# Performance work log

Hardware: AMD Instinct MI355X
Metric: run time of the kernel (lower is better)

Reference implementation:

```python
import jax, jax.numpy as jnp
import numpy as np

# Static config matching init_kwargs
H = 12            # num_heads
ALPHA = (1, 2, 3)
DEPTH = 5
BLOCK_DEPTH = 3
TOTAL_DEPTH_M1 = 14 - 1   # total_depth - 1
SMALL_ACTIVE = (BLOCK_DEPTH <= DEPTH <= TOTAL_DEPTH_M1 - BLOCK_DEPTH)  # True here


def _ln(x, g, b, eps=1e-5):
    m = jnp.mean(x, axis=-1, keepdims=True)
    v = jnp.mean((x - m) ** 2, axis=-1, keepdims=True)
    return (x - m) * jax.lax.rsqrt(v + eps) * g + b


def _attn_branch(xp, w_qkv, w_proj, b_proj, keep_heads, keep_ch):
    # xp: (B2, N, C). Heads >= keep_heads are zeroed in q,k,v (as in the torch
    # clone+zero), output channels >= keep_ch zeroed after proj.
    B2, N, C = xp.shape
    hd = C // H
    scale = hd ** -0.5
    qkv = (xp @ w_qkv).reshape(B2, N, 3, H, hd).transpose(2, 0, 3, 1, 4)  # (3,B2,H,N,hd)
    hmask = (jnp.arange(H) < keep_heads).astype(xp.dtype)[None, :, None, None]
    q, k, v = qkv[0] * hmask, qkv[1] * hmask, qkv[2] * hmask
    a = jax.nn.softmax(jnp.einsum('bhnd,bhmd->bhnm', q, k) * scale, axis=-1)
    o = jnp.einsum('bhnm,bhmd->bhnd', a, v).transpose(0, 2, 1, 3).reshape(B2, N, C)
    o = o @ w_proj + b_proj
    cmask = (jnp.arange(C) < keep_ch).astype(xp.dtype)
    return o * cmask


def _mlp_branch(xp, w1, b1, w2, b2, keep_ch):
    # Input channels >= keep_ch zeroed before fc1, output channels zeroed after fc2.
    C = xp.shape[-1]
    cmask = (jnp.arange(C) < keep_ch).astype(xp.dtype)
    h = jax.nn.gelu((xp * cmask) @ w1 + b1, approximate=False)  # torch nn.GELU exact
    return ((h @ w2) + b2) * cmask


def setup_inputs() -> dict:
    key = jax.random.key(0)
    ks = jax.random.split(key, 8)
    B, N, C = 64, 257, 768
    HID = 4 * C

    def w(k, shape):
        return jax.random.normal(k, shape, jnp.float32) * 0.02

    return {
        'x': jax.random.normal(ks[0], (B, N, C), jnp.float32),
        'gumbel_weights': jax.random.uniform(ks[1], (3,), jnp.float32),
        'n1l_g': jnp.ones((C,), jnp.float32), 'n1l_b': jnp.zeros((C,), jnp.float32),
        'n1s_g': jnp.ones((C,), jnp.float32), 'n1s_b': jnp.zeros((C,), jnp.float32),
        'w_qkv': w(ks[2], (C, 3 * C)),  # qkv_bias=False
        'w_proj': w(ks[3], (C, C)), 'b_proj': jnp.zeros((C,), jnp.float32),
        'n2l_g': jnp.ones((C,), jnp.float32), 'n2l_b': jnp.zeros((C,), jnp.float32),
        'n2s_g': jnp.ones((C,), jnp.float32), 'n2s_b': jnp.zeros((C,), jnp.float32),
        'w_fc1': w(ks[4], (C, HID)), 'b_fc1': jnp.zeros((HID,), jnp.float32),
        'w_fc2': w(ks[5], (HID, C)), 'b_fc2': jnp.zeros((C,), jnp.float32),
    }


def reference(x, gumbel_weights, n1l_g, n1l_b, n1s_g, n1s_b, w_qkv, w_proj, b_proj,
              n2l_g, n2l_b, n2s_g, n2s_b, w_fc1, b_fc1, w_fc2, b_fc2):
    B, N, C = x.shape
    B2 = B // 2

    # --- attention sub-block (pre-norm, residual) ---
    nl = _ln(x[:B2], n1l_g, n1l_b)
    ns = _ln(x[B2:], n1s_g, n1s_b)
    a_large = _attn_branch(nl, w_qkv, w_proj, b_proj, H, C)
    if SMALL_ACTIVE:
        a_small = sum(
            gumbel_weights[i] * _attn_branch(ns, w_qkv, w_proj, b_proj,
                                             H // ALPHA[i], C // ALPHA[i])
            for i in range(3))
        attn_out = jnp.concatenate([a_large, a_small], axis=0)
    else:
        attn_out = jnp.concatenate([a_large, a_large], axis=0)
    x = x + attn_out  # drop_path = Identity

    # --- mlp sub-block (pre-norm, residual) ---
    nl2 = _ln(x[:B2], n2l_g, n2l_b)
    ns2 = _ln(x[B2:], n2s_g, n2s_b)
    m_large = _mlp_branch(nl2, w_fc1, b_fc1, w_fc2, b_fc2, C)
    if SMALL_ACTIVE:
        m_small = sum(
            gumbel_weights[i] * _mlp_branch(ns2, w_fc1, b_fc1, w_fc2, b_fc2,
                                            C // ALPHA[i])
            for i in range(3))
        mlp_out = jnp.concatenate([m_large, m_small], axis=0)
    else:
        mlp_out = jnp.concatenate([m_large, m_large], axis=0)
    return x + mlp_out
```

## Files before the change

kernel.cpp:

```cpp
#include <hip/hip_runtime.h>
#include <hip/hip_bf16.h>

typedef short v8s __attribute__((ext_vector_type(8)));
typedef float v4f __attribute__((ext_vector_type(4)));

#define B2ROWS 8224
#define ROWS   16448

__device__ __forceinline__ float fast_gelu(float z) {
  float u = z * 0.70710678118654752f;
  float a = fabsf(u);
  float t = __builtin_amdgcn_rcpf(1.0f + 0.3275911f * a);
  float p = t * (0.254829592f + t * (-0.284496736f + t * (1.421413741f +
            t * (-1.453152027f + t * 1.061405429f))));
  float e = __expf(-a * a);
  float erfa = 1.0f - p * e;
  float erfu = copysignf(erfa, u);
  return 0.5f * z * (1.0f + erfu);
}

__global__ __launch_bounds__(256) void wprep(const float* __restrict__ W,
                                             __hip_bfloat16* __restrict__ Wt,
                                             int K, int N, int variant,
                                             const float* __restrict__ gw) {
  int k = blockIdx.x * 256 + threadIdx.x;
  int n = blockIdx.y;
  if (k >= K) return;
  float v = W[(size_t)k * N + n];
  if (variant == 1) {
    int h = k >> 6;
    float s = gw[0];
    if (h < 6 && n < 384) s += gw[1];
    if (h < 4 && n < 256) s += gw[2];
    v *= s;
  }
  Wt[(size_t)n * K + k] = __float2bfloat16(v);
}

__global__ void bias_prep(const float* __restrict__ bp, const float* __restrict__ b2,
                          const float* __restrict__ gw,
                          float* __restrict__ b_small, float* __restrict__ b2_small) {
  int c = blockIdx.x * 256 + threadIdx.x;
  if (c >= 768) return;
  float s = gw[0] + (c < 384 ? gw[1] : 0.f) + (c < 256 ? gw[2] : 0.f);
  b_small[c] = bp[c] * s;
  b2_small[c] = b2[c] * s;
}

__global__ __launch_bounds__(256) void ln_k(const float* __restrict__ X,
                                            __hip_bfloat16* __restrict__ out,
                                            const float* __restrict__ gl, const float* __restrict__ bl,
                                            const float* __restrict__ gs, const float* __restrict__ bs) {
  int wave = threadIdx.x >> 6, lane = threadIdx.x & 63;
  int row = blockIdx.x * 4 + wave;
  const float* g = (row < B2ROWS) ? gl : gs;
  const float* b = (row < B2ROWS) ? bl : bs;
  const float* xr = X + (size_t)row * 768;
  float v[12]; float s = 0.f, ss = 0.f;
#pragma unroll
  for (int i = 0; i < 12; i++) { v[i] = xr[lane + i * 64]; s += v[i]; ss += v[i] * v[i]; }
#pragma unroll
  for (int o = 32; o > 0; o >>= 1) { s += __shfl_xor(s, o, 64); ss += __shfl_xor(ss, o, 64); }
  float mean = s * (1.0f / 768.0f);
  float var = ss * (1.0f / 768.0f) - mean * mean;
  float rstd = rsqrtf(var + 1e-5f);
  __hip_bfloat16* orow = out + (size_t)row * 768;
#pragma unroll
  for (int i = 0; i < 12; i++) {
    int c = lane + i * 64;
    orow[c] = __float2bfloat16((v[i] - mean) * rstd * g[c] + b[c]);
  }
}

template<int FUSED>
__device__ __forceinline__ void gemm_body(
    const __hip_bfloat16* __restrict__ A, int lda,
    const __hip_bfloat16* __restrict__ Bt, int ldb,
    int M, int K,
    const float* __restrict__ bias,
    const float* __restrict__ resid, int ldr,
    const float* __restrict__ gw, int gidx,
    const __hip_bfloat16* __restrict__ addin,
    void* __restrict__ out, int ldo,
    int mode,
    __hip_bfloat16* __restrict__ aux1,
    __hip_bfloat16* __restrict__ aux2) {
  __shared__ __attribute__((aligned(16))) short Asm[3][128 * 32];
  __shared__ __attribute__((aligned(16))) short Bsm[3][128 * 32];
  int tid = threadIdx.x;
  int lane = tid & 63;
  int wave = tid >> 6;
  int wm = wave >> 1, wn = wave & 1;
  int l16 = lane & 15, quad = lane >> 4;

  int gx = gridDim.x;
  int nwg = gx * gridDim.y;
  int bid = blockIdx.y * gx + blockIdx.x;
  int q8 = nwg >> 3, r8 = nwg & 7;
  int xcd = bid & 7, lid = bid >> 3;
  int nb = (xcd < r8 ? xcd * (q8 + 1) : r8 * (q8 + 1) + (xcd - r8) * q8) + lid;
  int m0 = (nb / gx) * 128, n0 = (nb % gx) * 128;

  int sw = (quad ^ ((l16 >> 1) & 3)) * 8;

  const __hip_bfloat16* Ause = A;
  if (!FUSED && mode == 4) {
    if (n0 < 256) Ause = aux2;
    else if (n0 < 384) Ause = aux1;
    mode = 2;
  }

  int r4 = lane >> 2;
  int qs = (lane & 3) ^ ((r4 >> 1) & 3);

  const ushort* Au = (const ushort*)Ause;
  const ushort* Bu = (const ushort*)Bt;

  const ushort* agp[2];
  const ushort* bgp[2];
  int lof[2];
#pragma unroll
  for (int it = 0; it < 2; it++) {
    int rbase = wave * 16 + it * 64;
    int gr = m0 + rbase + r4; if (gr > M - 1) gr = M - 1;
    agp[it] = Au + (size_t)gr * lda + qs * 8;
    int gn = n0 + rbase + r4;
    bgp[it] = Bu + (size_t)gn * ldb + qs * 8;
    lof[it] = rbase * 32;
  }

  v4f acc[4][4];
#pragma unroll
  for (int i = 0; i < 4; i++)
#pragma unroll
    for (int j = 0; j < 4; j++) acc[i][j] = (v4f){0.f, 0.f, 0.f, 0.f};

  float bias4[4];
  float gw0 = 0.f, gw1 = 0.f, gw2 = 0.f;
  uint g1p[4][4][2], g2p[4][4][2];
  if constexpr (FUSED) {
    gw0 = gw[0]; gw1 = gw[1]; gw2 = gw[2];
#pragma unroll
    for (int j = 0; j < 4; j++) bias4[j] = bias[n0 + wn * 64 + j * 16 + l16];
  }

  auto snap = [&](uint (&gp)[4][4][2], float gwX) {
#pragma unroll
    for (int i = 0; i < 4; i++)
#pragma unroll
      for (int j = 0; j < 4; j++)
#pragma unroll
        for (int p = 0; p < 2; p++) {
          float v0 = gwX * fast_gelu(acc[i][j][2 * p] + bias4[j]);
          float v1 = gwX * fast_gelu(acc[i][j][2 * p + 1] + bias4[j]);
          __hip_bfloat16 h0 = __float2bfloat16(v0);
          __hip_bfloat16 h1 = __float2bfloat16(v1);
          gp[i][j][p] = ((uint)*(const ushort*)&h1 << 16) | (uint)*(const ushort*)&h0;
        }
  };

  auto stage = [&](int buf, int ko) {
#pragma unroll
    for (int it = 0; it < 2; it++) {
      __builtin_amdgcn_global_load_lds(
          (const __attribute__((address_space(1))) uint32_t*)(uintptr_t)(const void*)(agp[it] + ko),
          (__attribute__((address_space(3))) uint32_t*)(uint32_t)(uintptr_t)(const void*)&Asm[buf][lof[it]],
          16, 0, 0);
      __builtin_amdgcn_global_load_lds(
          (const __attribute__((address_space(1))) uint32_t*)(uintptr_t)(const void*)(bgp[it] + ko),
          (__attribute__((address_space(3))) uint32_t*)(uint32_t)(uintptr_t)(const void*)&Bsm[buf][lof[it]],
          16, 0, 0);
    }
  };

  int nk = K >> 5;
  stage(0, 0);
  stage(1, 32);

  int bc = 0;
  for (int t = 0; t < nk; ++t) {
    if constexpr (FUSED) {
      if (t == 8)  snap(g2p, gw2);
      if (t == 12) snap(g1p, gw1);
    }
    __builtin_amdgcn_sched_barrier(0);
    if (t + 1 < nk) {
      asm volatile("s_waitcnt vmcnt(4)" ::: "memory");
    } else {
      asm volatile("s_waitcnt vmcnt(0)" ::: "memory");
    }
    __builtin_amdgcn_s_barrier();
    __builtin_amdgcn_sched_barrier(0);
    if (t + 2 < nk) {
      int bsg = bc - 1; if (bsg < 0) bsg += 3;
      stage(bsg, (t + 2) * 32);
    }
    v8s af[4], bfr[4];
#pragma unroll
    for (int i = 0; i < 4; i++) af[i] = *(const v8s*)&Asm[bc][(wm * 64 + i * 16 + l16) * 32 + sw];
#pragma unroll
    for (int j = 0; j < 4; j++) bfr[j] = *(const v8s*)&Bsm[bc][(wn * 64 + j * 16 + l16) * 32 + sw];
#pragma unroll
    for (int i = 0; i < 4; i++)
#pragma unroll
      for (int j = 0; j < 4; j++)
        acc[i][j] = __builtin_amdgcn_mfma_f32_16x16x32_bf16(af[i], bfr[j], acc[i][j], 0, 0, 0);
    bc++; if (bc == 3) bc = 0;
  }

  if constexpr (FUSED) {
#pragma unroll
    for (int i = 0; i < 4; i++)
#pragma unroll
      for (int j = 0; j < 4; j++)
#pragma unroll
        for (int r = 0; r < 4; r++)
          acc[i][j][r] = gw0 * fast_gelu(acc[i][j][r] + bias4[j]);

    __syncthreads();
    ushort* S16 = (ushort*)(((wave < 2) ? (char*)Asm : (char*)Bsm) + (wave & 1) * 12288);

    auto flush = [&](void* dst) {
      asm volatile("s_waitcnt lgkmcnt(0)" ::: "memory");
#pragma unroll
      for (int i = 0; i < 4; i++)
#pragma unroll
        for (int j = 0; j < 4; j++)
#pragma unroll
          for (int r = 0; r < 4; r++) {
            __hip_bfloat16 hb = __float2bfloat16(acc[i][j][r]);
            S16[(i * 16 + quad * 4 + r) * 72 + j * 16 + l16] = *(const ushort*)&hb;
          }
      asm volatile("s_waitcnt lgkmcnt(0)" ::: "memory");
#pragma unroll
      for (int rr = 0; rr < 8; rr++) {
        int row = rr * 8 + (lane >> 3);
        int col0 = (lane & 7) * 8;
        int gr = m0 + wm * 64 + row;
        v8s val = *(const v8s*)&S16[row * 72 + col0];
        if (gr < M)
          *(v8s*)&((ushort*)dst)[(size_t)gr * ldo + (n0 + wn * 64 + col0)] = val;
      }
    };

    flush(out);
#pragma unroll
    for (int i = 0; i < 4; i++)
#pragma unroll
      for (int j = 0; j < 4; j++)
#pragma unroll
        for (int p = 0; p < 2; p++) {
          uint u = g1p[i][j][p];
          acc[i][j][2 * p]     += __uint_as_float(u << 16);
          acc[i][j][2 * p + 1] += __uint_as_float(u & 0xffff0000u);
        }
    flush(aux1);
#pragma unroll
    for (int i = 0; i < 4; i++)
#pragma unroll
      for (int j = 0; j < 4; j++)
#pragma unroll
        for (int p = 0; p < 2; p++) {
          uint u = g2p[i][j][p];
          acc[i][j][2 * p]     += __uint_as_float(u << 16);
          acc[i][j][2 * p + 1] += __uint_as_float(u & 0xffff0000u);
        }
    flush(aux2);
    return;
  } else {

  float scale = (gidx >= 0) ? gw[gidx] : 1.0f;

  __syncthreads();
  char* sbase = ((wave < 2) ? (char*)Asm : (char*)Bsm) + (wave & 1) * 12288;

  if (mode != 2) {
    ushort* S16 = (ushort*)sbase;
#pragma unroll
    for (int i = 0; i < 4; i++) {
#pragma unroll
      for (int j = 0; j < 4; j++) {
        int gc = n0 + wn * 64 + j * 16 + l16;
#pragma unroll
        for (int r = 0; r < 4; r++) {
          float v = acc[i][j][r];
          if (mode == 1) {
            float z = v + bias[gc];
            v = scale * fast_gelu(z);
          }
          __hip_bfloat16 hb = __float2bfloat16(v);
          S16[(i * 16 + quad * 4 + r) * 72 + j * 16 + l16] = *(const ushort*)&hb;
        }
      }
    }
    asm volatile("s_waitcnt lgkmcnt(0)" ::: "memory");
#pragma unroll
    for (int rr = 0; rr < 8; rr++) {
      int row = rr * 8 + (lane >> 3);
      int col0 = (lane & 7) * 8;
      int gr = m0 + wm * 64 + row;
      v8s val = *(const v8s*)&S16[row * 72 + col0];
      if (gr < M) {
        size_t go = (size_t)gr * ldo + (n0 + wn * 64 + col0);
        if (mode == 1 && addin) {
          v8s av = *(const v8s*)&((const ushort*)addin)[go];
#pragma unroll
          for (int e = 0; e < 8; e++) {
            float fv = __uint_as_float(((uint)(ushort)val[e]) << 16);
            float fa = __uint_as_float(((uint)(ushort)av[e]) << 16);
            __hip_bfloat16 hr = __float2bfloat16(fv + fa);
            val[e] = *(const short*)&hr;
          }
        }
        *(v8s*)&((ushort*)out)[go] = val;
      }
    }
  } else {
    float* S32 = (float*)sbase;
#pragma unroll
    for (int h = 0; h < 2; h++) {
      if (h) asm volatile("s_waitcnt lgkmcnt(0)" ::: "memory");
#pragma unroll
      for (int i = 0; i < 4; i++) {
#pragma unroll
        for (int jj = 0; jj < 2; jj++) {
          int j = h * 2 + jj;
          int gc = n0 + wn * 64 + j * 16 + l16;
#pragma unroll
          for (int r = 0; r < 4; r++)
            S32[(i * 16 + quad * 4 + r) * 36 + jj * 16 + l16] = acc[i][j][r] + bias[gc];
        }
      }
      asm volatile("s_waitcnt lgkmcnt(0)" ::: "memory");
#pragma unroll
      for (int rr = 0; rr < 8; rr++) {
        int row = rr * 8 + (lane >> 3);
        int c0 = (lane & 7) * 4;
        int gr = m0 + wm * 64 + row;
        v4f v = *(const v4f*)&S32[row * 36 + c0];
        if (gr < M) {
          int gc0 = n0 + wn * 64 + h * 32 + c0;
          v4f rv = *(const v4f*)&resid[(size_t)gr * ldr + gc0];
          v4f sres = v + rv;
          *(v4f*)&((float*)out)[(size_t)gr * ldo + gc0] = sres;
        }
      }
    }
  }
  }
}

__global__ __launch_bounds__(256) void gemm_k(
    const __hip_bfloat16* __restrict__ A, int lda,
    const __hip_bfloat16* __restrict__ Bt, int ldb,
    int M, int K,
    const float* __restrict__ bias,
    const float* __restrict__ resid, int ldr,
    const float* __restrict__ gw, int gidx,
    const __hip_bfloat16* __restrict__ addin,
    void* __restrict__ out, int ldo,
    int mode,
    __hip_bfloat16* __restrict__ aux1,
    __hip_bfloat16* __restrict__ aux2) {
  gemm_body<0>(A, lda, Bt, ldb, M, K, bias, resid, ldr, gw, gidx, addin,
               out, ldo, mode, aux1, aux2);
}

__global__ __launch_bounds__(256) void fc1f_k(
    const __hip_bfloat16* __restrict__ A, int lda,
    const __hip_bfloat16* __restrict__ Bt, int ldb,
    int M, int K,
    const float* __restrict__ bias,
    const float* __restrict__ gw,
    void* __restrict__ out, int ldo,
    __hip_bfloat16* __restrict__ outB,
    __hip_bfloat16* __restrict__ outC) {
  gemm_body<1>(A, lda, Bt, ldb, M, K, bias, nullptr, 0, gw, -1, nullptr,
               out, ldo, 3, outB, outC);
}

__global__ __launch_bounds__(256) void attn_k(const __hip_bfloat16* __restrict__ qkv,
                                              __hip_bfloat16* __restrict__ O) {
  __shared__ ushort Ks[64 * 72];
  __shared__ ushort Vs[64 * 64];
  __shared__ ushort Ps[4][16 * 72];
  int bh = blockIdx.x;
  int b = bh / 12, h = bh % 12;
  size_t base = (size_t)b * 257;
  const ushort* Qg = (const ushort*)qkv;
  int tid = threadIdx.x;
  int w = tid >> 6, lane = tid & 63;
  int l16 = lane & 15, quad = lane >> 4;
  int qrow0 = blockIdx.y * 64 + w * 16;

  v8s aq[2];
  {
    int gr = qrow0 + l16; if (gr > 256) gr = 256;
    const ushort* qp = Qg + (base + gr) * 2304 + h * 64;
    aq[0] = *(const v8s*)(qp + quad * 8);
    aq[1] = *(const v8s*)(qp + 32 + quad * 8);
  }

  float mrow[4], lrow[4];
  v4f o[4];
#pragma unroll
  for (int r = 0; r < 4; r++) { mrow[r] = -1e30f; lrow[r] = 0.f; }
#pragma unroll
  for (int dt = 0; dt < 4; dt++) o[dt] = (v4f){0.f, 0.f, 0.f, 0.f};

  for (int kt = 0; kt < 5; kt++) {
    __syncthreads();
#pragma unroll
    for (int it = 0; it < 2; it++) {
      int ch = tid + it * 256;
      int row = ch >> 3, oct = ch & 7;
      int gk = kt * 64 + row; if (gk > 256) gk = 256;
      *(uint4*)&Ks[row * 72 + oct * 8] =
        *(const uint4*)(Qg + (base + gk) * 2304 + 768 + h * 64 + oct * 8);
    }
#pragma unroll
    for (int it = 0; it < 2; it++) {
      int oct = w + it * 4;
      int gk = kt * 64 + lane; if (gk > 256) gk = 256;
      ushort tmp[8];
      *(uint4*)tmp = *(const uint4*)(Qg + (base + gk) * 2304 + 1536 + h * 64 + oct * 8);
#pragma unroll
      for (int j = 0; j < 8; j++) {
        int d = oct * 8 + j;
        Vs[d * 64 + (((lane >> 3) ^ j) * 8) + (lane & 7)] = tmp[j];
      }
    }
    __syncthreads();

    v4f s[4];
#pragma unroll
    for (int jt = 0; jt < 4; jt++) {
      v8s bk0 = *(const v8s*)&Ks[(jt * 16 + l16) * 72 + quad * 8];
      v8s bk1 = *(const v8s*)&Ks[(jt * 16 + l16) * 72 + 32 + quad * 8];
      v4f acc = (v4f){0.f, 0.f, 0.f, 0.f};
      acc = __builtin_amdgcn_mfma_f32_16x16x32_bf16(aq[0], bk0, acc, 0, 0, 0);
      acc = __builtin_amdgcn_mfma_f32_16x16x32_bf16(aq[1], bk1, acc, 0, 0, 0);
      s[jt] = acc;
    }
#pragma unroll
    for (int jt = 0; jt < 4; jt++) {
      int col = kt * 64 + jt * 16 + l16;
      bool valid = col < 257;
#pragma unroll
      for (int r = 0; r < 4; r++)
        s[jt][r] = valid ? s[jt][r] * 0.125f : -1e30f;
    }
    float mnew[4], alpha[4], psum[4];
#pragma unroll
    for (int r = 0; r < 4; r++) {
      float mx = fmaxf(fmaxf(s[0][r], s[1][r]), fmaxf(s[2][r], s[3][r]));
#pragma unroll
      for (int off = 1; off < 16; off <<= 1) mx = fmaxf(mx, __shfl_xor(mx, off, 64));
      mnew[r] = fmaxf(mrow[r], mx);
      alpha[r] = __expf(mrow[r] - mnew[r]);
      mrow[r] = mnew[r];
      psum[r] = 0.f;
    }
#pragma unroll
    for (int jt = 0; jt < 4; jt++) {
#pragma unroll
      for (int r = 0; r < 4; r++) {
        float p = __expf(s[jt][r] - mnew[r]);
        psum[r] += p;
        __hip_bfloat16 pb = __float2bfloat16(p);
        Ps[w][(quad * 4 + r) * 72 + jt * 16 + l16] = *(ushort*)&pb;
      }
    }
#pragma unroll
    for (int r = 0; r < 4; r++) {
#pragma unroll
      for (int off = 1; off < 16; off <<= 1) psum[r] += __shfl_xor(psum[r], off, 64);
      lrow[r] = lrow[r] * alpha[r] + psum[r];
    }
#pragma unroll
    for (int dt = 0; dt < 4; dt++)
#pragma unroll
      for (int r = 0; r < 4; r++) o[dt][r] *= alpha[r];
    v8s pa0 = *(const v8s*)&Ps[w][l16 * 72 + quad * 8];
    v8s pa1 = *(const v8s*)&Ps[w][l16 * 72 + 32 + quad * 8];
#pragma unroll
    for (int dt = 0; dt < 4; dt++) {
      int d = dt * 16 + l16;
      v8s bv0 = *(const v8s*)&Vs[d * 64 + ((quad ^ (d & 7)) * 8)];
      v8s bv1 = *(const v8s*)&Vs[d * 64 + (((4 + quad) ^ (d & 7)) * 8)];
      o[dt] = __builtin_amdgcn_mfma_f32_16x16x32_bf16(pa0, bv0, o[dt], 0, 0, 0);
      o[dt] = __builtin_amdgcn_mfma_f32_16x16x32_bf16(pa1, bv1, o[dt], 0, 0, 0);
    }
  }
#pragma unroll
  for (int r = 0; r < 4; r++) {
    int gr = qrow0 + quad * 4 + r;
    if (gr < 257) {
      float inv = 1.f / lrow[r];
      __hip_bfloat16* orow = O + (base + gr) * 768 + h * 64;
#pragma unroll
      for (int dt = 0; dt < 4; dt++)
        orow[dt * 16 + l16] = __float2bfloat16(o[dt][r] * inv);
    }
  }
}

extern "C" void kernel_launch(void* const* d_in, const int* in_sizes, int n_in,
                              void* d_out, int out_size, void* d_ws, size_t ws_size,
                              hipStream_t stream) {
  const float* x      = (const float*)d_in[0];
  const float* gw     = (const float*)d_in[1];
  const float* n1l_g  = (const float*)d_in[2];
  const float* n1l_b  = (const float*)d_in[3];
  const float* n1s_g  = (const float*)d_in[4];
  const float* n1s_b  = (const float*)d_in[5];
  const float* w_qkv  = (const float*)d_in[6];
  const float* w_proj = (const float*)d_in[7];
  const float* b_proj = (const float*)d_in[8];
  const float* n2l_g  = (const float*)d_in[9];
  const float* n2l_b  = (const float*)d_in[10];
  const float* n2s_g  = (const float*)d_in[11];
  const float* n2s_b  = (const float*)d_in[12];
  const float* w_fc1  = (const float*)d_in[13];
  const float* b_fc1  = (const float*)d_in[14];
  const float* w_fc2  = (const float*)d_in[15];
  const float* b_fc2  = (const float*)d_in[16];
  float* out = (float*)d_out;

  const size_t REQUIRED = (size_t)(2304*768 + 2*768*768 + 2*3072*768) * 2
                        + 2 * 768 * 4 + 512
                        + (size_t)ROWS * 768 * 2
                        + (size_t)ROWS * 2304 * 2;
  if (ws_size < REQUIRED) return;

  char* ws = (char*)d_ws;
  size_t off = 0;
  auto alloc = [&](size_t bytes) -> void* {
    void* p = ws + off;
    off = (off + bytes + 255) & ~(size_t)255;
    return p;
  };
  __hip_bfloat16* wqkv_t  = (__hip_bfloat16*)alloc((size_t)2304 * 768 * 2);
  __hip_bfloat16* wproj_l = (__hip_bfloat16*)alloc((size_t)768 * 768 * 2);
  __hip_bfloat16* wproj_s = (__hip_bfloat16*)alloc((size_t)768 * 768 * 2);
  __hip_bfloat16* wfc1_t  = (__hip_bfloat16*)alloc((size_t)3072 * 768 * 2);
  __hip_bfloat16* wfc2_t  = (__hip_bfloat16*)alloc((size_t)768 * 3072 * 2);
  float* b_small  = (float*)alloc(768 * 4);
  float* b2_small = (float*)alloc(768 * 4);
  __hip_bfloat16* xn   = (__hip_bfloat16*)alloc((size_t)ROWS * 768 * 2);
  __hip_bfloat16* qkv  = (__hip_bfloat16*)alloc((size_t)ROWS * 2304 * 2);
  __hip_bfloat16* Obuf = xn;
  __hip_bfloat16* xn2  = qkv;
  __hip_bfloat16* hbuf = qkv + (size_t)ROWS * 768;

  const size_t HB2 = (size_t)B2ROWS * 3072 * 2;
  bool roomy = ws_size >= REQUIRED + 2 * HB2 + 512;
  __hip_bfloat16 *outB = nullptr, *outC = nullptr;
  if (roomy) {
    outB = (__hip_bfloat16*)alloc(HB2);
    outC = (__hip_bfloat16*)alloc(HB2);
  }

  wprep<<<dim3(3, 2304), 256, 0, stream>>>(w_qkv, wqkv_t, 768, 2304, 0, gw);
  wprep<<<dim3(3, 768),  256, 0, stream>>>(w_proj, wproj_l, 768, 768, 0, gw);
  wprep<<<dim3(3, 768),  256, 0, stream>>>(w_proj, wproj_s, 768, 768, 1, gw);
  wprep<<<dim3(3, 3072), 256, 0, stream>>>(w_fc1, wfc1_t, 768, 3072, 0, gw);
  wprep<<<dim3(12, 768), 256, 0, stream>>>(w_fc2, wfc2_t, 3072, 768, 0, gw);
  bias_prep<<<3, 256, 0, stream>>>(b_proj, b_fc2, gw, b_small, b2_small);

  ln_k<<<ROWS / 4, 256, 0, stream>>>(x, xn, n1l_g, n1l_b, n1s_g, n1s_b);

  gemm_k<<<dim3(18, 129), 256, 0, stream>>>(xn, 768, wqkv_t, 768, ROWS, 768,
                                            nullptr, nullptr, 0, gw, -1, nullptr,
                                            qkv, 2304, 0, nullptr, nullptr);
  attn_k<<<dim3(768, 5), 256, 0, stream>>>(qkv, Obuf);

  gemm_k<<<dim3(6, 65), 256, 0, stream>>>(Obuf, 768, wproj_l, 768, B2ROWS, 768,
                                          b_proj, x, 768, gw, -1, nullptr, out, 768, 2,
                                          nullptr, nullptr);
  gemm_k<<<dim3(6, 65), 256, 0, stream>>>(Obuf + (size_t)B2ROWS * 768, 768, wproj_s, 768, B2ROWS, 768,
                                          b_small, x + (size_t)B2ROWS * 768, 768, gw, -1, nullptr,
                                          out + (size_t)B2ROWS * 768, 768, 2, nullptr, nullptr);

  ln_k<<<ROWS / 4, 256, 0, stream>>>(out, xn2, n2l_g, n2l_b, n2s_g, n2s_b);
  const __hip_bfloat16* xn2s = xn2 + (size_t)B2ROWS * 768;
  float* outs = out + (size_t)B2ROWS * 768;

  gemm_k<<<dim3(24, 65), 256, 0, stream>>>(xn2, 768, wfc1_t, 768, B2ROWS, 768,
                                           b_fc1, nullptr, 0, gw, -1, nullptr, hbuf, 3072, 1,
                                           nullptr, nullptr);
  gemm_k<<<dim3(6, 65), 256, 0, stream>>>(hbuf, 3072, wfc2_t, 3072, B2ROWS, 3072,
                                          b_fc2, out, 768, gw, -1, nullptr, out, 768, 2,
                                          nullptr, nullptr);

  if (roomy) {
    fc1f_k<<<dim3(24, 65), 256, 0, stream>>>(xn2s, 768, wfc1_t, 768, B2ROWS, 768,
                                             b_fc1, gw, hbuf, 3072, outB, outC);
    gemm_k<<<dim3(6, 65), 256, 0, stream>>>(hbuf, 3072, wfc2_t, 3072, B2ROWS, 3072,
                                            b2_small, outs, 768, gw, -1, nullptr, outs, 768, 4,
                                            outB, outC);
  } else {
    gemm_k<<<dim3(24, 65), 256, 0, stream>>>(xn2s, 768, wfc1_t, 768, B2ROWS, 768,
                                             b_fc1, nullptr, 0, gw, 0, nullptr, hbuf, 3072, 1,
                                             nullptr, nullptr);
    gemm_k<<<dim3(3, 65), 256, 0, stream>>>(hbuf, 3072, wfc2_t + (size_t)384 * 3072, 3072, B2ROWS, 3072,
                                            b2_small + 384, outs + 384, 768, gw, -1, nullptr, outs + 384, 768, 2,
                                            nullptr, nullptr);
    gemm_k<<<dim3(24, 65), 256, 0, stream>>>(xn2s, 768, wfc1_t, 768, B2ROWS, 384,
                                             b_fc1, nullptr, 0, gw, 1, hbuf, hbuf, 3072, 1,
                                             nullptr, nullptr);
    gemm_k<<<dim3(1, 65), 256, 0, stream>>>(hbuf, 3072, wfc2_t + (size_t)256 * 3072, 3072, B2ROWS, 3072,
                                            b2_small + 256, outs + 256, 768, gw, -1, nullptr, outs + 256, 768, 2,
                                            nullptr, nullptr);
    gemm_k<<<dim3(24, 65), 256, 0, stream>>>(xn2s, 768, wfc1_t, 768, B2ROWS, 256,
                                             b_fc1, nullptr, 0, gw, 2, hbuf, hbuf, 3072, 1,
                                             nullptr, nullptr);
    gemm_k<<<dim3(2, 65), 256, 0, stream>>>(hbuf, 3072, wfc2_t, 3072, B2ROWS, 3072,
                                            b2_small, outs, 768, gw, -1, nullptr, outs, 768, 2,
                                            nullptr, nullptr);
  }
}
```

Baseline: 745.2 us.

## Merge proj GEMMs into one launch and shrink fused fc1 tile width

The two attention output projection GEMMs (large and small branches) become a single launch with a new mode that picks the A, weight, bias, residual and output pointers from the row block index. This removes one launch and the tail effect between them. The fused fc1 kernel that keeps three GELU-scaled snapshots now uses 128x64 tiles instead of 128x128, which halves the accumulator and snapshot registers and doubles the grid. The aim is better occupancy and less register pressure, at the cost of lower reuse of each A tile.

Result: faster. 726.6 us (-2.5%).

```diff
diff --git a/kernel.cpp b/kernel.cpp
--- a/kernel.cpp
+++ b/kernel.cpp
@@ -2,6 +2,7 @@
 #include <hip/hip_bf16.h>
 
 typedef short v8s __attribute__((ext_vector_type(8)));
+typedef short v4s __attribute__((ext_vector_type(4)));
 typedef float v4f __attribute__((ext_vector_type(4)));
 
 #define B2ROWS 8224
@@ -72,284 +73,6 @@
   }
 }
 
-template<int FUSED>
-__device__ __forceinline__ void gemm_body(
-    const __hip_bfloat16* __restrict__ A, int lda,
-    const __hip_bfloat16* __restrict__ Bt, int ldb,
-    int M, int K,
-    const float* __restrict__ bias,
-    const float* __restrict__ resid, int ldr,
-    const float* __restrict__ gw, int gidx,
-    const __hip_bfloat16* __restrict__ addin,
-    void* __restrict__ out, int ldo,
-    int mode,
-    __hip_bfloat16* __restrict__ aux1,
-    __hip_bfloat16* __restrict__ aux2) {
-  __shared__ __attribute__((aligned(16))) short Asm[3][128 * 32];
-  __shared__ __attribute__((aligned(16))) short Bsm[3][128 * 32];
-  int tid = threadIdx.x;
-  int lane = tid & 63;
-  int wave = tid >> 6;
-  int wm = wave >> 1, wn = wave & 1;
-  int l16 = lane & 15, quad = lane >> 4;
-
-  int gx = gridDim.x;
-  int nwg = gx * gridDim.y;
-  int bid = blockIdx.y * gx + blockIdx.x;
-  int q8 = nwg >> 3, r8 = nwg & 7;
-  int xcd = bid & 7, lid = bid >> 3;
-  int nb = (xcd < r8 ? xcd * (q8 + 1) : r8 * (q8 + 1) + (xcd - r8) * q8) + lid;
-  int m0 = (nb / gx) * 128, n0 = (nb % gx) * 128;
-
-  int sw = (quad ^ ((l16 >> 1) & 3)) * 8;
-
-  const __hip_bfloat16* Ause = A;
-  if (!FUSED && mode == 4) {
-    if (n0 < 256) Ause = aux2;
-    else if (n0 < 384) Ause = aux1;
-    mode = 2;
-  }
-
-  int r4 = lane >> 2;
-  int qs = (lane & 3) ^ ((r4 >> 1) & 3);
-
-  const ushort* Au = (const ushort*)Ause;
-  const ushort* Bu = (const ushort*)Bt;
-
-  const ushort* agp[2];
-  const ushort* bgp[2];
-  int lof[2];
-#pragma unroll
-  for (int it = 0; it < 2; it++) {
-    int rbase = wave * 16 + it * 64;
-    int gr = m0 + rbase + r4; if (gr > M - 1) gr = M - 1;
-    agp[it] = Au + (size_t)gr * lda + qs * 8;
-    int gn = n0 + rbase + r4;
-    bgp[it] = Bu + (size_t)gn * ldb + qs * 8;
-    lof[it] = rbase * 32;
-  }
-
-  v4f acc[4][4];
-#pragma unroll
-  for (int i = 0; i < 4; i++)
-#pragma unroll
-    for (int j = 0; j < 4; j++) acc[i][j] = (v4f){0.f, 0.f, 0.f, 0.f};
-
-  float bias4[4];
-  float gw0 = 0.f, gw1 = 0.f, gw2 = 0.f;
-  uint g1p[4][4][2], g2p[4][4][2];
-  if constexpr (FUSED) {
-    gw0 = gw[0]; gw1 = gw[1]; gw2 = gw[2];
-#pragma unroll
-    for (int j = 0; j < 4; j++) bias4[j] = bias[n0 + wn * 64 + j * 16 + l16];
-  }
-
-  auto snap = [&](uint (&gp)[4][4][2], float gwX) {
-#pragma unroll
-    for (int i = 0; i < 4; i++)
-#pragma unroll
-      for (int j = 0; j < 4; j++)
-#pragma unroll
-        for (int p = 0; p < 2; p++) {
-          float v0 = gwX * fast_gelu(acc[i][j][2 * p] + bias4[j]);
-          float v1 = gwX * fast_gelu(acc[i][j][2 * p + 1] + bias4[j]);
-          __hip_bfloat16 h0 = __float2bfloat16(v0);
-          __hip_bfloat16 h1 = __float2bfloat16(v1);
-          gp[i][j][p] = ((uint)*(const ushort*)&h1 << 16) | (uint)*(const ushort*)&h0;
-        }
-  };
-
-  auto stage = [&](int buf, int ko) {
-#pragma unroll
-    for (int it = 0; it < 2; it++) {
-      __builtin_amdgcn_global_load_lds(
-          (const __attribute__((address_space(1))) uint32_t*)(uintptr_t)(const void*)(agp[it] + ko),
-          (__attribute__((address_space(3))) uint32_t*)(uint32_t)(uintptr_t)(const void*)&Asm[buf][lof[it]],
-          16, 0, 0);
-      __builtin_amdgcn_global_load_lds(
-          (const __attribute__((address_space(1))) uint32_t*)(uintptr_t)(const void*)(bgp[it] + ko),
-          (__attribute__((address_space(3))) uint32_t*)(uint32_t)(uintptr_t)(const void*)&Bsm[buf][lof[it]],
-          16, 0, 0);
-    }
-  };
-
-  int nk = K >> 5;
-  stage(0, 0);
-  stage(1, 32);
-
-  int bc = 0;
-  for (int t = 0; t < nk; ++t) {
-    if constexpr (FUSED) {
-      if (t == 8)  snap(g2p, gw2);
-      if (t == 12) snap(g1p, gw1);
-    }
-    __builtin_amdgcn_sched_barrier(0);
-    if (t + 1 < nk) {
-      asm volatile("s_waitcnt vmcnt(4)" ::: "memory");
-    } else {
-      asm volatile("s_waitcnt vmcnt(0)" ::: "memory");
-    }
-    __builtin_amdgcn_s_barrier();
-    __builtin_amdgcn_sched_barrier(0);
-    if (t + 2 < nk) {
-      int bsg = bc - 1; if (bsg < 0) bsg += 3;
-      stage(bsg, (t + 2) * 32);
-    }
-    v8s af[4], bfr[4];
-#pragma unroll
-    for (int i = 0; i < 4; i++) af[i] = *(const v8s*)&Asm[bc][(wm * 64 + i * 16 + l16) * 32 + sw];
-#pragma unroll
-    for (int j = 0; j < 4; j++) bfr[j] = *(const v8s*)&Bsm[bc][(wn * 64 + j * 16 + l16) * 32 + sw];
-#pragma unroll
-    for (int i = 0; i < 4; i++)
-#pragma unroll
-      for (int j = 0; j < 4; j++)
-        acc[i][j] = __builtin_amdgcn_mfma_f32_16x16x32_bf16(af[i], bfr[j], acc[i][j], 0, 0, 0);
-    bc++; if (bc == 3) bc = 0;
-  }
-
-  if constexpr (FUSED) {
-#pragma unroll
-    for (int i = 0; i < 4; i++)
-#pragma unroll
-      for (int j = 0; j < 4; j++)
-#pragma unroll
-        for (int r = 0; r < 4; r++)
-          acc[i][j][r] = gw0 * fast_gelu(acc[i][j][r] + bias4[j]);
-
-    __syncthreads();
-    ushort* S16 = (ushort*)(((wave < 2) ? (char*)Asm : (char*)Bsm) + (wave & 1) * 12288);
-
-    auto flush = [&](void* dst) {
-      asm volatile("s_waitcnt lgkmcnt(0)" ::: "memory");
-#pragma unroll
-      for (int i = 0; i < 4; i++)
-#pragma unroll
-        for (int j = 0; j < 4; j++)
-#pragma unroll
-          for (int r = 0; r < 4; r++) {
-            __hip_bfloat16 hb = __float2bfloat16(acc[i][j][r]);
-            S16[(i * 16 + quad * 4 + r) * 72 + j * 16 + l16] = *(const ushort*)&hb;
-          }
-      asm volatile("s_waitcnt lgkmcnt(0)" ::: "memory");
-#pragma unroll
-      for (int rr = 0; rr < 8; rr++) {
-        int row = rr * 8 + (lane >> 3);
-        int col0 = (lane & 7) * 8;
-        int gr = m0 + wm * 64 + row;
-        v8s val = *(const v8s*)&S16[row * 72 + col0];
-        if (gr < M)
-          *(v8s*)&((ushort*)dst)[(size_t)gr * ldo + (n0 + wn * 64 + col0)] = val;
-      }
-    };
-
-    flush(out);
-#pragma unroll
-    for (int i = 0; i < 4; i++)
-#pragma unroll
-      for (int j = 0; j < 4; j++)
-#pragma unroll
-        for (int p = 0; p < 2; p++) {
-          uint u = g1p[i][j][p];
-          acc[i][j][2 * p]     += __uint_as_float(u << 16);
-          acc[i][j][2 * p + 1] += __uint_as_float(u & 0xffff0000u);
-        }
-    flush(aux1);
-#pragma unroll
-    for (int i = 0; i < 4; i++)
-#pragma unroll
-      for (int j = 0; j < 4; j++)
-#pragma unroll
-        for (int p = 0; p < 2; p++) {
-          uint u = g2p[i][j][p];
-          acc[i][j][2 * p]     += __uint_as_float(u << 16);
-          acc[i][j][2 * p + 1] += __uint_as_float(u & 0xffff0000u);
-        }
-    flush(aux2);
-    return;
-  } else {
-
-  float scale = (gidx >= 0) ? gw[gidx] : 1.0f;
-
-  __syncthreads();
-  char* sbase = ((wave < 2) ? (char*)Asm : (char*)Bsm) + (wave & 1) * 12288;
-
-  if (mode != 2) {
-    ushort* S16 = (ushort*)sbase;
-#pragma unroll
-    for (int i = 0; i < 4; i++) {
-#pragma unroll
-      for (int j = 0; j < 4; j++) {
-        int gc = n0 + wn * 64 + j * 16 + l16;
-#pragma unroll
-        for (int r = 0; r < 4; r++) {
-          float v = acc[i][j][r];
-          if (mode == 1) {
-            float z = v + bias[gc];
-            v = scale * fast_gelu(z);
-          }
-          __hip_bfloat16 hb = __float2bfloat16(v);
-          S16[(i * 16 + quad * 4 + r) * 72 + j * 16 + l16] = *(const ushort*)&hb;
-        }
-      }
-    }
-    asm volatile("s_waitcnt lgkmcnt(0)" ::: "memory");
-#pragma unroll
-    for (int rr = 0; rr < 8; rr++) {
-      int row = rr * 8 + (lane >> 3);
-      int col0 = (lane & 7) * 8;
-      int gr = m0 + wm * 64 + row;
-      v8s val = *(const v8s*)&S16[row * 72 + col0];
-      if (gr < M) {
-        size_t go = (size_t)gr * ldo + (n0 + wn * 64 + col0);
-        if (mode == 1 && addin) {
-          v8s av = *(const v8s*)&((const ushort*)addin)[go];
-#pragma unroll
-          for (int e = 0; e < 8; e++) {
-            float fv = __uint_as_float(((uint)(ushort)val[e]) << 16);
-            float fa = __uint_as_float(((uint)(ushort)av[e]) << 16);
-            __hip_bfloat16 hr = __float2bfloat16(fv + fa);
-            val[e] = *(const short*)&hr;
-          }
-        }
-        *(v8s*)&((ushort*)out)[go] = val;
-      }
-    }
-  } else {
-    float* S32 = (float*)sbase;
-#pragma unroll
-    for (int h = 0; h < 2; h++) {
-      if (h) asm volatile("s_waitcnt lgkmcnt(0)" ::: "memory");
-#pragma unroll
-      for (int i = 0; i < 4; i++) {
-#pragma unroll
-        for (int jj = 0; jj < 2; jj++) {
-          int j = h * 2 + jj;
-          int gc = n0 + wn * 64 + j * 16 + l16;
-#pragma unroll
-          for (int r = 0; r < 4; r++)
-            S32[(i * 16 + quad * 4 + r) * 36 + jj * 16 + l16] = acc[i][j][r] + bias[gc];
-        }
-      }
-      asm volatile("s_waitcnt lgkmcnt(0)" ::: "memory");
-#pragma unroll
-      for (int rr = 0; rr < 8; rr++) {
-        int row = rr * 8 + (lane >> 3);
-        int c0 = (lane & 7) * 4;
-        int gr = m0 + wm * 64 + row;
-        v4f v = *(const v4f*)&S32[row * 36 + c0];
-        if (gr < M) {
-          int gc0 = n0 + wn * 64 + h * 32 + c0;
-          v4f rv = *(const v4f*)&resid[(size_t)gr * ldr + gc0];
-          v4f sres = v + rv;
-          *(v4f*)&((float*)out)[(size_t)gr * ldo + gc0] = sres;
-        }
-      }
-    }
-  }
-  }
-}
-
 __global__ __launch_bounds__(256) void gemm_k(
     const __hip_bfloat16* __restrict__ A, int lda,
     const __hip_bfloat16* __restrict__ Bt, int ldb,
@@ -360,10 +83,196 @@
     const __hip_bfloat16* __restrict__ addin,
     void* __restrict__ out, int ldo,
     int mode,
-    __hip_bfloat16* __restrict__ aux1,
-    __hip_bfloat16* __restrict__ aux2) {
-  gemm_body<0>(A, lda, Bt, ldb, M, K, bias, resid, ldr, gw, gidx, addin,
-               out, ldo, mode, aux1, aux2);
+    const __hip_bfloat16* __restrict__ aux1,
+    const __hip_bfloat16* __restrict__ aux2,
+    const float* __restrict__ bias2) {
+  __shared__ __attribute__((aligned(16))) short Asm[3][128 * 32];
+  __shared__ __attribute__((aligned(16))) short Bsm[3][128 * 32];
+  int tid = threadIdx.x;
+  int lane = tid & 63;
+  int wave = tid >> 6;
+  int wm = wave >> 1, wn = wave & 1;
+  int l16 = lane & 15, quad = lane >> 4;
+
+  int gx = gridDim.x;
+  int nwg = gx * gridDim.y;
+  int bid = blockIdx.y * gx + blockIdx.x;
+  int q8 = nwg >> 3, r8 = nwg & 7;
+  int xcd = bid & 7, lid = bid >> 3;
+  int nb = (xcd < r8 ? xcd * (q8 + 1) : r8 * (q8 + 1) + (xcd - r8) * q8) + lid;
+  int m0 = (nb / gx) * 128, n0 = (nb % gx) * 128;
+
+  int sw = (quad ^ ((l16 >> 1) & 3)) * 8;
+
+  const __hip_bfloat16* Ause = A;
+  const __hip_bfloat16* Btuse = Bt;
+  const float* bias_u = bias;
+  const float* resid_u = resid;
+  void* out_u = out;
+  if (mode == 4) {
+    if (n0 < 256) Ause = aux2;
+    else if (n0 < 384) Ause = aux1;
+    mode = 2;
+  } else if (mode == 5) {
+    if (m0 >= 8320) {
+      m0 -= 8320;
+      Ause = A + (size_t)B2ROWS * lda;
+      Btuse = aux1;
+      bias_u = bias2;
+      resid_u = resid + (size_t)B2ROWS * ldr;
+      out_u = (void*)((float*)out + (size_t)B2ROWS * ldo);
+    }
+    mode = 2;
+  }
+
+  int r4 = lane >> 2;
+  int qs = (lane & 3) ^ ((r4 >> 1) & 3);
+
+  const ushort* Au = (const ushort*)Ause;
+  const ushort* Bu = (const ushort*)Btuse;
+
+  const ushort* agp[2];
+  const ushort* bgp[2];
+  int lof[2];
+#pragma unroll
+  for (int it = 0; it < 2; it++) {
+    int rbase = wave * 16 + it * 64;
+    int gr = m0 + rbase + r4; if (gr > M - 1) gr = M - 1;
+    agp[it] = Au + (size_t)gr * lda + qs * 8;
+    int gn = n0 + rbase + r4;
+    bgp[it] = Bu + (size_t)gn * ldb + qs * 8;
+    lof[it] = rbase * 32;
+  }
+
+  v4f acc[4][4];
+#pragma unroll
+  for (int i = 0; i < 4; i++)
+#pragma unroll
+    for (int j = 0; j < 4; j++) acc[i][j] = (v4f){0.f, 0.f, 0.f, 0.f};
+
+  auto stage = [&](int buf, int ko) {
+#pragma unroll
+    for (int it = 0; it < 2; it++) {
+      __builtin_amdgcn_global_load_lds(
+          (const __attribute__((address_space(1))) uint32_t*)(uintptr_t)(const void*)(agp[it] + ko),
+          (__attribute__((address_space(3))) uint32_t*)(uint32_t)(uintptr_t)(const void*)&Asm[buf][lof[it]],
+          16, 0, 0);
+      __builtin_amdgcn_global_load_lds(
+          (const __attribute__((address_space(1))) uint32_t*)(uintptr_t)(const void*)(bgp[it] + ko),
+          (__attribute__((address_space(3))) uint32_t*)(uint32_t)(uintptr_t)(const void*)&Bsm[buf][lof[it]],
+          16, 0, 0);
+    }
+  };
+
+  int nk = K >> 5;
+  stage(0, 0);
+  stage(1, 32);
+
+  int bc = 0;
+  for (int t = 0; t < nk; ++t) {
+    __builtin_amdgcn_sched_barrier(0);
+    if (t + 1 < nk) {
+      asm volatile("s_waitcnt vmcnt(4)" ::: "memory");
+    } else {
+      asm volatile("s_waitcnt vmcnt(0)" ::: "memory");
+    }
+    __builtin_amdgcn_s_barrier();
+    __builtin_amdgcn_sched_barrier(0);
+    if (t + 2 < nk) {
+      int bsg = bc - 1; if (bsg < 0) bsg += 3;
+      stage(bsg, (t + 2) * 32);
+    }
+    v8s af[4], bfr[4];
+#pragma unroll
+    for (int i = 0; i < 4; i++) af[i] = *(const v8s*)&Asm[bc][(wm * 64 + i * 16 + l16) * 32 + sw];
+#pragma unroll
+    for (int j = 0; j < 4; j++) bfr[j] = *(const v8s*)&Bsm[bc][(wn * 64 + j * 16 + l16) * 32 + sw];
+#pragma unroll
+    for (int i = 0; i < 4; i++)
+#pragma unroll
+      for (int j = 0; j < 4; j++)
+        acc[i][j] = __builtin_amdgcn_mfma_f32_16x16x32_bf16(af[i], bfr[j], acc[i][j], 0, 0, 0);
+    bc++; if (bc == 3) bc = 0;
+  }
+
+  float scale = (gidx >= 0) ? gw[gidx] : 1.0f;
+
+  __syncthreads();
+  char* sbase = ((wave < 2) ? (char*)Asm : (char*)Bsm) + (wave & 1) * 12288;
+
+  if (mode != 2) {
+    ushort* S16 = (ushort*)sbase;
+#pragma unroll
+    for (int i = 0; i < 4; i++) {
+#pragma unroll
+      for (int j = 0; j < 4; j++) {
+        int gc = n0 + wn * 64 + j * 16 + l16;
+#pragma unroll
+        for (int r = 0; r < 4; r++) {
+          float v = acc[i][j][r];
+          if (mode == 1) {
+            float z = v + bias_u[gc];
+            v = scale * fast_gelu(z);
+          }
+          __hip_bfloat16 hb = __float2bfloat16(v);
+          S16[(i * 16 + quad * 4 + r) * 72 + j * 16 + l16] = *(const ushort*)&hb;
+        }
+      }
+    }
+    asm volatile("s_waitcnt lgkmcnt(0)" ::: "memory");
+#pragma unroll
+    for (int rr = 0; rr < 8; rr++) {
+      int row = rr * 8 + (lane >> 3);
+      int col0 = (lane & 7) * 8;
+      int gr = m0 + wm * 64 + row;
+      v8s val = *(const v8s*)&S16[row * 72 + col0];
+      if (gr < M) {
+        size_t go = (size_t)gr * ldo + (n0 + wn * 64 + col0);
+        if (mode == 1 && addin) {
+          v8s av = *(const v8s*)&((const ushort*)addin)[go];
+#pragma unroll
+          for (int e = 0; e < 8; e++) {
+            float fv = __uint_as_float(((uint)(ushort)val[e]) << 16);
+            float fa = __uint_as_float(((uint)(ushort)av[e]) << 16);
+            __hip_bfloat16 hr = __float2bfloat16(fv + fa);
+            val[e] = *(const short*)&hr;
+          }
+        }
+        *(v8s*)&((ushort*)out_u)[go] = val;
+      }
+    }
+  } else {
+    float* S32 = (float*)sbase;
+#pragma unroll
+    for (int h = 0; h < 2; h++) {
+      if (h) asm volatile("s_waitcnt lgkmcnt(0)" ::: "memory");
+#pragma unroll
+      for (int i = 0; i < 4; i++) {
+#pragma unroll
+        for (int jj = 0; jj < 2; jj++) {
+          int j = h * 2 + jj;
+          int gc = n0 + wn * 64 + j * 16 + l16;
+#pragma unroll
+          for (int r = 0; r < 4; r++)
+            S32[(i * 16 + quad * 4 + r) * 36 + jj * 16 + l16] = acc[i][j][r] + bias_u[gc];
+        }
+      }
+      asm volatile("s_waitcnt lgkmcnt(0)" ::: "memory");
+#pragma unroll
+      for (int rr = 0; rr < 8; rr++) {
+        int row = rr * 8 + (lane >> 3);
+        int c0 = (lane & 7) * 4;
+        int gr = m0 + wm * 64 + row;
+        v4f v = *(const v4f*)&S32[row * 36 + c0];
+        if (gr < M) {
+          int gc0 = n0 + wn * 64 + h * 32 + c0;
+          v4f rv = *(const v4f*)&resid_u[(size_t)gr * ldr + gc0];
+          v4f sres = v + rv;
+          *(v4f*)&((float*)out_u)[(size_t)gr * ldo + gc0] = sres;
+        }
+      }
+    }
+  }
 }
 
 __global__ __launch_bounds__(256) void fc1f_k(
@@ -375,8 +284,166 @@
     void* __restrict__ out, int ldo,
     __hip_bfloat16* __restrict__ outB,
     __hip_bfloat16* __restrict__ outC) {
-  gemm_body<1>(A, lda, Bt, ldb, M, K, bias, nullptr, 0, gw, -1, nullptr,
-               out, ldo, 3, outB, outC);
+  __shared__ __attribute__((aligned(16))) short As2[3][128 * 32];
+  __shared__ __attribute__((aligned(16))) short Bs2[3][64 * 32];
+  int tid = threadIdx.x, lane = tid & 63, wave = tid >> 6;
+  int wm = wave >> 1, wn = wave & 1;
+  int l16 = lane & 15, quad = lane >> 4;
+
+  int gx = gridDim.x;
+  int nwg = gx * gridDim.y;
+  int bid = blockIdx.y * gx + blockIdx.x;
+  int q8 = nwg >> 3, r8 = nwg & 7;
+  int xcd = bid & 7, lid = bid >> 3;
+  int nb = (xcd < r8 ? xcd * (q8 + 1) : r8 * (q8 + 1) + (xcd - r8) * q8) + lid;
+  int m0 = (nb / gx) * 128, n0 = (nb % gx) * 64;
+
+  int sw = (quad ^ ((l16 >> 1) & 3)) * 8;
+  int r4 = lane >> 2;
+  int qs = (lane & 3) ^ ((r4 >> 1) & 3);
+
+  const ushort* Au = (const ushort*)A;
+  const ushort* Bu = (const ushort*)Bt;
+  const ushort* agp[2];
+#pragma unroll
+  for (int it = 0; it < 2; it++) {
+    int gr = m0 + wave * 16 + it * 64 + r4; if (gr > M - 1) gr = M - 1;
+    agp[it] = Au + (size_t)gr * lda + qs * 8;
+  }
+  const ushort* bgp = Bu + (size_t)(n0 + wave * 16 + r4) * ldb + qs * 8;
+
+  v4f acc[4][2];
+#pragma unroll
+  for (int i = 0; i < 4; i++)
+#pragma unroll
+    for (int j = 0; j < 2; j++) acc[i][j] = (v4f){0.f, 0.f, 0.f, 0.f};
+
+  float gw0 = gw[0], gw1 = gw[1], gw2 = gw[2];
+  float bias2r[2];
+#pragma unroll
+  for (int j = 0; j < 2; j++) bias2r[j] = bias[n0 + wn * 32 + j * 16 + l16];
+
+  uint g1p[4][2][2], g2p[4][2][2];
+
+  auto snap = [&](uint (&gp)[4][2][2], float gwX) {
+#pragma unroll
+    for (int i = 0; i < 4; i++)
+#pragma unroll
+      for (int j = 0; j < 2; j++)
+#pragma unroll
+        for (int p = 0; p < 2; p++) {
+          float v0 = gwX * fast_gelu(acc[i][j][2 * p] + bias2r[j]);
+          float v1 = gwX * fast_gelu(acc[i][j][2 * p + 1] + bias2r[j]);
+          __hip_bfloat16 h0 = __float2bfloat16(v0);
+          __hip_bfloat16 h1 = __float2bfloat16(v1);
+          gp[i][j][p] = ((uint)*(const ushort*)&h1 << 16) | (uint)*(const ushort*)&h0;
+        }
+  };
+
+  auto stage = [&](int buf, int ko) {
+#pragma unroll
+    for (int it = 0; it < 2; it++) {
+      __builtin_amdgcn_global_load_lds(
+          (const __attribute__((address_space(1))) uint32_t*)(uintptr_t)(const void*)(agp[it] + ko),
+          (__attribute__((address_space(3))) uint32_t*)(uint32_t)(uintptr_t)(const void*)&As2[buf][(wave * 16 + it * 64) * 32],
+          16, 0, 0);
+    }
+    __builtin_amdgcn_global_load_lds(
+        (const __attribute__((address_space(1))) uint32_t*)(uintptr_t)(const void*)(bgp + ko),
+        (__attribute__((address_space(3))) uint32_t*)(uint32_t)(uintptr_t)(const void*)&Bs2[buf][(wave * 16) * 32],
+        16, 0, 0);
+  };
+
+  int nk = K >> 5;
+  stage(0, 0);
+  stage(1, 32);
+
+  int bc = 0;
+  for (int t = 0; t < nk; ++t) {
+    if (t == 8)  snap(g2p, gw2);
+    if (t == 12) snap(g1p, gw1);
+    __builtin_amdgcn_sched_barrier(0);
+    if (t + 1 < nk) {
+      asm volatile("s_waitcnt vmcnt(3)" ::: "memory");
+    } else {
+      asm volatile("s_waitcnt vmcnt(0)" ::: "memory");
+    }
+    __builtin_amdgcn_s_barrier();
+    __builtin_amdgcn_sched_barrier(0);
+    if (t + 2 < nk) {
+      int bsg = bc - 1; if (bsg < 0) bsg += 3;
+      stage(bsg, (t + 2) * 32);
+    }
+    v8s af[4], bfr[2];
+#pragma unroll
+    for (int i = 0; i < 4; i++) af[i] = *(const v8s*)&As2[bc][(wm * 64 + i * 16 + l16) * 32 + sw];
+#pragma unroll
+    for (int j = 0; j < 2; j++) bfr[j] = *(const v8s*)&Bs2[bc][(wn * 32 + j * 16 + l16) * 32 + sw];
+#pragma unroll
+    for (int i = 0; i < 4; i++)
+#pragma unroll
+      for (int j = 0; j < 2; j++)
+        acc[i][j] = __builtin_amdgcn_mfma_f32_16x16x32_bf16(af[i], bfr[j], acc[i][j], 0, 0, 0);
+    bc++; if (bc == 3) bc = 0;
+  }
+
+#pragma unroll
+  for (int i = 0; i < 4; i++)
+#pragma unroll
+    for (int j = 0; j < 2; j++)
+#pragma unroll
+      for (int r = 0; r < 4; r++)
+        acc[i][j][r] = gw0 * fast_gelu(acc[i][j][r] + bias2r[j]);
+
+  __syncthreads();
+  ushort* S = (ushort*)As2 + wave * 2560;
+
+  auto flush = [&](void* dst) {
+    asm volatile("s_waitcnt lgkmcnt(0)" ::: "memory");
+#pragma unroll
+    for (int i = 0; i < 4; i++)
+#pragma unroll
+      for (int j = 0; j < 2; j++)
+#pragma unroll
+        for (int r = 0; r < 4; r++) {
+          __hip_bfloat16 hb = __float2bfloat16(acc[i][j][r]);
+          S[(i * 16 + quad * 4 + r) * 40 + j * 16 + l16] = *(const ushort*)&hb;
+        }
+    asm volatile("s_waitcnt lgkmcnt(0)" ::: "memory");
+#pragma unroll
+    for (int rr = 0; rr < 8; rr++) {
+      int row = rr * 8 + (lane >> 3);
+      int col0 = (lane & 7) * 4;
+      int gr = m0 + wm * 64 + row;
+      v4s val = *(const v4s*)&S[row * 40 + col0];
+      if (gr < M)
+        *(v4s*)&((ushort*)dst)[(size_t)gr * ldo + (n0 + wn * 32 + col0)] = val;
+    }
+  };
+
+  flush(out);
+#pragma unroll
+  for (int i = 0; i < 4; i++)
+#pragma unroll
+    for (int j = 0; j < 2; j++)
+#pragma unroll
+      for (int p = 0; p < 2; p++) {
+        uint u = g1p[i][j][p];
+        acc[i][j][2 * p]     += __uint_as_float(u << 16);
+        acc[i][j][2 * p + 1] += __uint_as_float(u & 0xffff0000u);
+      }
+  flush(outB);
+#pragma unroll
+  for (int i = 0; i < 4; i++)
+#pragma unroll
+    for (int j = 0; j < 2; j++)
+#pragma unroll
+      for (int p = 0; p < 2; p++) {
+        uint u = g2p[i][j][p];
+        acc[i][j][2 * p]     += __uint_as_float(u << 16);
+        acc[i][j][2 * p + 1] += __uint_as_float(u & 0xffff0000u);
+      }
+  flush(outC);
 }
 
 __global__ __launch_bounds__(256) void attn_k(const __hip_bfloat16* __restrict__ qkv,
@@ -572,15 +639,12 @@
 
   gemm_k<<<dim3(18, 129), 256, 0, stream>>>(xn, 768, wqkv_t, 768, ROWS, 768,
                                             nullptr, nullptr, 0, gw, -1, nullptr,
-                                            qkv, 2304, 0, nullptr, nullptr);
+                                            qkv, 2304, 0, nullptr, nullptr, nullptr);
   attn_k<<<dim3(768, 5), 256, 0, stream>>>(qkv, Obuf);
 
-  gemm_k<<<dim3(6, 65), 256, 0, stream>>>(Obuf, 768, wproj_l, 768, B2ROWS, 768,
-                                          b_proj, x, 768, gw, -1, nullptr, out, 768, 2,
-                                          nullptr, nullptr);
-  gemm_k<<<dim3(6, 65), 256, 0, stream>>>(Obuf + (size_t)B2ROWS * 768, 768, wproj_s, 768, B2ROWS, 768,
-                                          b_small, x + (size_t)B2ROWS * 768, 768, gw, -1, nullptr,
-                                          out + (size_t)B2ROWS * 768, 768, 2, nullptr, nullptr);
+  gemm_k<<<dim3(6, 130), 256, 0, stream>>>(Obuf, 768, wproj_l, 768, B2ROWS, 768,
+                                           b_proj, x, 768, gw, -1, nullptr, out, 768, 5,
+                                           wproj_s, nullptr, b_small);
 
   ln_k<<<ROWS / 4, 256, 0, stream>>>(out, xn2, n2l_g, n2l_b, n2s_g, n2s_b);
   const __hip_bfloat16* xn2s = xn2 + (size_t)B2ROWS * 768;
@@ -588,35 +652,35 @@
 
   gemm_k<<<dim3(24, 65), 256, 0, stream>>>(xn2, 768, wfc1_t, 768, B2ROWS, 768,
                                            b_fc1, nullptr, 0, gw, -1, nullptr, hbuf, 3072, 1,
-                                           nullptr, nullptr);
+                                           nullptr, nullptr, nullptr);
   gemm_k<<<dim3(6, 65), 256, 0, stream>>>(hbuf, 3072, wfc2_t, 3072, B2ROWS, 3072,
                                           b_fc2, out, 768, gw, -1, nullptr, out, 768, 2,
-                                          nullptr, nullptr);
+                                          nullptr, nullptr, nullptr);
 
   if (roomy) {
-    fc1f_k<<<dim3(24, 65), 256, 0, stream>>>(xn2s, 768, wfc1_t, 768, B2ROWS, 768,
+    fc1f_k<<<dim3(48, 65), 256, 0, stream>>>(xn2s, 768, wfc1_t, 768, B2ROWS, 768,
                                              b_fc1, gw, hbuf, 3072, outB, outC);
     gemm_k<<<dim3(6, 65), 256, 0, stream>>>(hbuf, 3072, wfc2_t, 3072, B2ROWS, 3072,
                                             b2_small, outs, 768, gw, -1, nullptr, outs, 768, 4,
-                                            outB, outC);
+                                            outB, outC, nullptr);
   } else {
     gemm_k<<<dim3(24, 65), 256, 0, stream>>>(xn2s, 768, wfc1_t, 768, B2ROWS, 768,
                                              b_fc1, nullptr, 0, gw, 0, nullptr, hbuf, 3072, 1,
-                                             nullptr, nullptr);
+                                             nullptr, nullptr, nullptr);
     gemm_k<<<dim3(3, 65), 256, 0, stream>>>(hbuf, 3072, wfc2_t + (size_t)384 * 3072, 3072, B2ROWS, 3072,
                                             b2_small + 384, outs + 384, 768, gw, -1, nullptr, outs + 384, 768, 2,
-                                            nullptr, nullptr);
+                                            nullptr, nullptr, nullptr);
     gemm_k<<<dim3(24, 65), 256, 0, stream>>>(xn2s, 768, wfc1_t, 768, B2ROWS, 384,
                                              b_fc1, nullptr, 0, gw, 1, hbuf, hbuf, 3072, 1,
-                                             nullptr, nullptr);
+                                             nullptr, nullptr, nullptr);
     gemm_k<<<dim3(1, 65), 256, 0, stream>>>(hbuf, 3072, wfc2_t + (size_t)256 * 3072, 3072, B2ROWS, 3072,
                                             b2_small + 256, outs + 256, 768, gw, -1, nullptr, outs + 256, 768, 2,
-                                            nullptr, nullptr);
+                                            nullptr, nullptr, nullptr);
     gemm_k<<<dim3(24, 65), 256, 0, stream>>>(xn2s, 768, wfc1_t, 768, B2ROWS, 256,
                                              b_fc1, nullptr, 0, gw, 2, hbuf, hbuf, 3072, 1,
-                                             nullptr, nullptr);
+                                             nullptr, nullptr, nullptr);
     gemm_k<<<dim3(2, 65), 256, 0, stream>>>(hbuf, 3072, wfc2_t, 3072, B2ROWS, 3072,
                                             b2_small, outs, 768, gw, -1, nullptr, outs, 768, 2,
-                                            nullptr, nullptr);
-  }
-}
+                                            nullptr, nullptr, nullptr);
+  }
+}
```
